# Kernel optimization log

Measured on AMD Instinct MI355X. Metric: run time of the kernel, lower is better.

Reference implementation:

```python
import jax, jax.numpy as jnp
import numpy as np

# ---- static physical configuration (matches init_kwargs param dict) ----
NX = NY = 513
NL = 3
N_ENS = 4
LX = LY = 5120.0e3
DX = LX / (NX - 1)
DY = LY / (NY - 1)
F0 = 9.375e-5
BETA = 1.754e-11
A2 = 0.0
A4 = 2.0e9
DELTA_EK = 2.0
TAU0 = 2.0e-5
BCCO = 0.2
ZFBC = BCCO / (1.0 + 0.5 * BCCO)
DT = 600.0
NUM_STEPS = 4
HEIGHTS = np.array([350.0, 750.0, 2900.0])
RED_G = np.array([0.025, 0.0125])

JAC_COEF = 1.0 / (F0 * DX * DY)
HYPERDIFF_COEF = A4 / F0**2 / DX**6
BOTTOM_FRICTION_COEF = DELTA_EK / (2.0 * abs(F0) * DX**2 * (-HEIGHTS[-1]))


def _build_constants():
    """Precompute stratification / mode / Helmholtz matrices (float64 numpy, cast to f32)."""
    A = np.zeros((NL, NL))
    A[0, 0] = 1.0 / (HEIGHTS[0] * RED_G[0])
    A[0, 1] = -1.0 / (HEIGHTS[0] * RED_G[0])
    for i in range(1, NL - 1):
        A[i, i - 1] = -1.0 / (HEIGHTS[i] * RED_G[i - 1])
        A[i, i] = 1.0 / HEIGHTS[i] * (1.0 / RED_G[i] + 1.0 / RED_G[i - 1])
        A[i, i + 1] = -1.0 / (HEIGHTS[i] * RED_G[i])
    A[-1, -1] = 1.0 / (HEIGHTS[NL - 1] * RED_G[NL - 2])
    A[-1, -2] = -1.0 / (HEIGHTS[NL - 1] * RED_G[NL - 2])
    lam_r, R = np.linalg.eig(A)
    lam_l, L = np.linalg.eig(A.T)
    lam_r, R, lam_l, L = lam_r.real, R.real, lam_l.real, L.real
    # align left eigenvectors with right eigenvalue ordering (biorthogonality)
    order = np.array([int(np.argmin(np.abs(lam_l - lr))) for lr in lam_r])
    L = L[:, order]
    Cl2m = np.diag(1.0 / np.diag(L.T @ R)) @ L.T
    Cm2l = R
    lambd = lam_r
    # DST-I eigenvalues of the 5-point Laplacian on the interior grid
    xg, yg = np.meshgrid(np.arange(1, NX - 1), np.arange(1, NY - 1), indexing='ij')
    lap_dst = (2 * (np.cos(np.pi / (NX - 1) * xg) - 1) / DX**2
               + 2 * (np.cos(np.pi / (NY - 1) * yg) - 1) / DY**2)
    helm_dst = lap_dst[None] / F0**2 - lambd[:, None, None]  # (nl, nx-2, ny-2)

    def np_dstI1D(x):
        N = x.shape[-1]
        xp = np.zeros(x.shape[:-1] + (N + 2,))
        xp[..., 1:-1] = x
        return np.fft.irfft(-1j * xp, n=2 * (N + 1), axis=-1, norm='ortho')[..., 1:N + 1]

    def np_dstI2D(x):
        return np.swapaxes(np_dstI1D(np.swapaxes(np_dstI1D(x), -1, -2)), -1, -2)

    const = np.ones((NL, NX, NY)) / (NX * NY)
    s = np.zeros_like(const)
    s[:, 1:-1, 1:-1] = np_dstI2D(np_dstI2D(const[:, 1:-1, 1:-1]) / helm_dst)
    hom_sol = (const + s * lambd[:, None, None])[:-1]  # (nl-1, nx, ny)
    M = (Cm2l[1:] - Cm2l[:-1])[:NL - 1, :NL - 1] * hom_sol.mean((1, 2))[None, :]
    alpha = -np.linalg.inv(M) @ (Cm2l[1:, :-1] - Cm2l[:-1, :-1])
    # wind forcing: curl(tau)/(f0*H1) on interior points; tau_y = 0, tau_x(y) only
    tau_x = -TAU0 * np.cos(2 * np.pi * (np.arange(NY) + 0.5) / NY)[None, :] * np.ones((NX, NY))
    dtaux_dy = (tau_x[1:-1, 2:] - tau_x[1:-1, :-2]) / (2 * DY)
    wind = (-dtaux_dy / (F0 * HEIGHTS[0]))[None]  # (1, nx-2, ny-2)
    f32 = lambda a: jnp.asarray(a, jnp.float32)
    return dict(A=f32(A), Cl2m=f32(Cl2m), Cm2l=f32(Cm2l), helmoltz_dst=f32(helm_dst),
                alpha_matrix=f32(alpha), homogeneous_sol=f32(hom_sol), wind_forcing=f32(wind))


# ---------------- stencil ops ----------------

def _pad11(x):
    return jnp.pad(x, [(0, 0)] * (x.ndim - 2) + [(1, 1), (1, 1)])


def laplacian_h_nobc(f):
    # unscaled 5-point Laplacian, interior values only: (..., nx-2, ny-2)
    return (f[..., 2:, 1:-1] + f[..., :-2, 1:-1] + f[..., 1:-1, 2:] + f[..., 1:-1, :-2]
            - 4.0 * f[..., 1:-1, 1:-1])


def laplacian_h(f, fc):
    # full-grid Laplacian with partial-slip boundary treatment (coefficient fc = zfbc)
    lap = _pad11(laplacian_h_nobc(f))
    lap = lap.at[..., 0, :].set(fc * (f[..., 1, :] - f[..., 0, :]))
    lap = lap.at[..., -1, :].set(fc * (f[..., -2, :] - f[..., -1, :]))
    lap = lap.at[..., :, 0].set(fc * (f[..., :, 1] - f[..., :, 0]))
    lap = lap.at[..., :, -1].set(fc * (f[..., :, -2] - f[..., :, -1]))
    return lap


def laplacian_h_boundaries(f, fc):
    # boundary Laplacian values, concat order: x=0 (y interior), x=-1, y=0 (full x), y=-1
    return jnp.concatenate([
        fc * (f[..., 1, 1:-1] - f[..., 0, 1:-1]),
        fc * (f[..., -2, 1:-1] - f[..., -1, 1:-1]),
        fc * (f[..., :, 1] - f[..., :, 0]),
        fc * (f[..., :, -2] - f[..., :, -1])], axis=-1)


def jacobi_h(f, g):
    # Arakawa 9-point Jacobian J(f, g), interior values (..., nx-2, ny-2)
    dx_f = f[..., 2:, :] - f[..., :-2, :]
    dx_g = g[..., 2:, :] - g[..., :-2, :]
    dy_f = f[..., 2:] - f[..., :-2]
    dy_g = g[..., 2:] - g[..., :-2]
    return ((dx_f[..., 1:-1] * dy_g[..., 1:-1, :] - dx_g[..., 1:-1] * dy_f[..., 1:-1, :])
            + (f[..., 2:, 1:-1] * dy_g[..., 2:, :] - f[..., :-2, 1:-1] * dy_g[..., :-2, :])
            - (f[..., 1:-1, 2:] * dx_g[..., 2:] - f[..., 1:-1, :-2] * dx_g[..., :-2])
            + (g[..., 1:-1, 2:] * dx_f[..., 2:] - g[..., 1:-1, :-2] * dx_f[..., :-2])
            - (g[..., 2:, 1:-1] * dy_f[..., 2:, :] - g[..., :-2, 1:-1] * dy_f[..., :-2, :])) / 12.0


# ---------------- DST-I elliptic solve ----------------

def dstI1D(x):
    N = x.shape[-1]
    z = jnp.zeros(x.shape[:-1] + (1,), x.dtype)
    xp = jnp.concatenate([z, x, z], axis=-1)
    return jnp.fft.irfft(-1j * xp.astype(jnp.complex64), n=2 * (N + 1), axis=-1,
                         norm='ortho')[..., 1:N + 1]


def dstI2D(x):
    return jnp.swapaxes(dstI1D(jnp.swapaxes(dstI1D(x), -1, -2)), -1, -2)


def inverse_elliptic_dst(f, op_dst):
    return dstI2D(dstI2D(f) / op_dst)


# ---------------- QG time derivative ----------------

def _time_derivatives(y, A, Cl2m, Cm2l, helm_dst, alpha, hom_sol, wind):
    q, p = y[0], y[1]  # (..., nl, nx, ny)
    # advection + hyperdiffusion RHS on interior (a_2 == 0 branch skipped as in source)
    rhs = JAC_COEF * jacobi_h(q, p)
    delta2_p = laplacian_h(p, ZFBC)
    rhs = rhs - HYPERDIFF_COEF * laplacian_h_nobc(laplacian_h(delta2_p, ZFBC))
    rhs = rhs.at[..., 0:1, :, :].add(wind)
    rhs = rhs.at[..., -1:, :, :].add(BOTTOM_FRICTION_COEF * laplacian_h_nobc(p[..., -1:, :, :]))
    dq = _pad11(rhs)
    # layers -> modes, DST Helmholtz inversion, homogeneous-solution correction
    rhs_h = jnp.einsum('ij,...jxy->...ixy', Cl2m, dq)
    dp_modes = _pad11(inverse_elliptic_dst(rhs_h[..., 1:-1, 1:-1], helm_dst))
    mean_m = dp_modes[..., :-1, :, :].mean((-2, -1))  # (..., nl-1)
    dalpha = jnp.einsum('ij,...j->...i', alpha, mean_m)[..., None, None]
    dp_modes = dp_modes.at[..., :-1, :, :].add(dalpha * hom_sol)
    dp = jnp.einsum('ij,...jxy->...ixy', Cm2l, dp_modes)
    # boundary vorticity update
    dp_bound = jnp.concatenate([dp[..., 0, 1:-1], dp[..., -1, 1:-1],
                                dp[..., :, 0], dp[..., :, -1]], axis=-1)
    delta_p_bound = laplacian_h_boundaries(dp / (F0 * DX)**2, ZFBC)
    dq_bound = delta_p_bound - jnp.einsum('ij,...jl->...il', A, dp_bound)
    ny2 = NY - 2
    dq = dq.at[..., 0, 1:-1].set(dq_bound[..., :ny2])
    dq = dq.at[..., -1, 1:-1].set(dq_bound[..., ny2:2 * ny2])
    dq = dq.at[..., :, 0].set(dq_bound[..., 2 * ny2:2 * ny2 + NX])
    dq = dq.at[..., :, -1].set(dq_bound[..., 2 * ny2 + NX:2 * ny2 + 2 * NX])
    return jnp.stack((dq, dp), 0)


def _forecast(y0, t, A, Cl2m, Cm2l, helm_dst, alpha, hom_sol, wind):
    deriv = lambda y: _time_derivatives(y, A, Cl2m, Cm2l, helm_dst, alpha, hom_sol, wind)

    def step(y, dt_):
        k1 = deriv(y)
        k2 = deriv(y + 0.5 * dt_ * k1)
        k3 = deriv(y + 0.5 * dt_ * k2)
        k4 = deriv(y + dt_ * k3)
        y_next = y + (dt_ / 6.0) * (k1 + 2.0 * k2 + 2.0 * k3 + k4)
        return y_next, y_next

    _, traj = jax.lax.scan(step, y0, t[1:] - t[:-1])
    return jnp.concatenate([y0[None], traj], axis=0)  # (T, 2, n_ens, nl, nx, ny)


def setup_inputs() -> dict:
    key = jax.random.key(0)
    y0 = 0.1 * jax.random.normal(key, (2, N_ENS, NL, NX, NY), dtype=jnp.float32)
    t = jnp.arange(NUM_STEPS + 1, dtype=jnp.float32) * DT
    consts = _build_constants()
    return dict(y0=y0, t=t, **consts)


def reference(y0, t, A, Cl2m, Cm2l, helmoltz_dst, alpha_matrix, homogeneous_sol, wind_forcing):
    return _forecast(y0, t, A, Cl2m, Cm2l, helmoltz_dst, alpha_matrix,
                     homogeneous_sol, wind_forcing)
```

## Files before the change

### kernel.cpp

```cpp
#include <hip/hip_runtime.h>
#include <math.h>

#define NXY 513
#define NIN 511
#define NL3 3
#define NE4 4
#define NB 12
#define GLD 512

static constexpr long FS  = (long)NE4 * NL3 * NXY * NXY;
static constexpr long GSZ = (long)NB * GLD * GLD;
static constexpr int  NSTEPS = 4;

static constexpr double dF0 = 9.375e-05;
static constexpr double dDX = 10000.0;
static constexpr float ZFBCf     = (float)(0.2 / (1.0 + 0.5 * 0.2));
static constexpr float JACCf     = (float)(1.0 / (dF0 * dDX * dDX));
static constexpr float HYPCf     = (float)(2.0e9 / (dF0 * dF0) / (dDX*dDX*dDX*dDX*dDX*dDX));
static constexpr float BFCf      = (float)(2.0 / (2.0 * dF0 * dDX * dDX * (-2900.0)));
static constexpr float INVF0DX2f = (float)(1.0 / ((dF0 * dDX) * (dF0 * dDX)));

typedef short  bf16x8 __attribute__((ext_vector_type(8)));
typedef float  f32x4  __attribute__((ext_vector_type(4)));
typedef unsigned int u32;
typedef __attribute__((address_space(1))) const u32 GAS;
typedef __attribute__((address_space(3))) u32 LAS;
#define GLDS(gp, lp) __builtin_amdgcn_global_load_lds((GAS*)(gp), (LAS*)(lp), 16, 0, 0)

__device__ __forceinline__ unsigned short f2bf(float x) {
    unsigned int u = __float_as_uint(x);
    return (unsigned short)((u + 0x7FFFu + ((u >> 16) & 1u)) >> 16);
}
__device__ __forceinline__ float bf2f(unsigned short h) {
    return __uint_as_float(((unsigned int)h) << 16);
}

__global__ void initS_kernel(unsigned short* __restrict__ Sh, unsigned short* __restrict__ Sl) {
    int k = blockIdx.x * 256 + threadIdx.x;
    int n = blockIdx.y;
    if (k >= GLD || n >= GLD) return;
    float v = 0.f;
    if (n < NIN && k < NIN) {
        int m = ((n + 1) * (k + 1)) & 1023;
        v = (float)(0.0625 * sin(M_PI * (double)m / 512.0));
    }
    unsigned short hs = f2bf(v);
    Sh[n * GLD + k] = hs;
    Sl[n * GLD + k] = f2bf(v - bf2f(hs));
}

__global__ __launch_bounds__(256) void fused_rhs_l2m(
    float* __restrict__ kq, unsigned short* __restrict__ Gh, unsigned short* __restrict__ Gl,
    const float* __restrict__ y, const float* __restrict__ wind, const float* __restrict__ Cl2m)
{
    __shared__ float ps[22][72];
    __shared__ float qs[22][72];
    __shared__ float l1[22][72];
    __shared__ float l2[22][72];
    const int e  = blockIdx.z;
    const int x0 = 1 + blockIdx.y * 16;
    const int y0 = 1 + blockIdx.x * 64;
    const int t  = threadIdx.x;
    const float* q = y;
    const float* p = y + FS;
    float rhs[4][3];

#define LAPBC(a, i, j, gx, gy) \
    ((gy) == 0       ? ZFBCf * (a[i][(j)+1] - a[i][j]) : \
     (gy) == NXY-1   ? ZFBCf * (a[i][(j)-1] - a[i][j]) : \
     (gx) == 0       ? ZFBCf * (a[(i)+1][j] - a[i][j]) : \
     (gx) == NXY-1   ? ZFBCf * (a[(i)-1][j] - a[i][j]) : \
     a[(i)+1][j] + a[(i)-1][j] + a[i][(j)+1] + a[i][(j)-1] - 4.f * a[i][j])

#pragma unroll
    for (int l = 0; l < 3; ++l) {
        __syncthreads();
        const int c = e * NL3 + l;
        const size_t off = (size_t)c * NXY * NXY;
        const float* pp = p + off;
        const float* qp = q + off;
        for (int idx = t; idx < 22 * 70; idx += 256) {
            int i = idx / 70, j = idx % 70;
            int gx = x0 - 3 + i, gy = y0 - 3 + j;
            bool in = (gx >= 0 && gx < NXY && gy >= 0 && gy < NXY);
            size_t go = (size_t)gx * NXY + gy;
            ps[i][j] = in ? pp[go] : 0.f;
            qs[i][j] = in ? qp[go] : 0.f;
        }
        __syncthreads();
        for (int idx = t; idx < 20 * 68; idx += 256) {
            int i = 1 + idx / 68, j = 1 + idx % 68;
            int gx = x0 - 3 + i, gy = y0 - 3 + j;
            float v = 0.f;
            if (gx >= 0 && gx < NXY && gy >= 0 && gy < NXY) v = LAPBC(ps, i, j, gx, gy);
            l1[i][j] = v;
        }
        __syncthreads();
        for (int idx = t; idx < 18 * 66; idx += 256) {
            int i = 2 + idx / 66, j = 2 + idx % 66;
            int gx = x0 - 3 + i, gy = y0 - 3 + j;
            float v = 0.f;
            if (gx >= 0 && gx < NXY && gy >= 0 && gy < NXY) v = LAPBC(l1, i, j, gx, gy);
            l2[i][j] = v;
        }
        __syncthreads();
#pragma unroll
        for (int u = 0; u < 4; ++u) {
            int idx = t + 256 * u;
            int i = 3 + idx / 64, j = 3 + idx % 64;
            int gx = x0 - 3 + i, gy = y0 - 3 + j;
            if (gx > NIN || gy > NIN) { rhs[u][l] = 0.f; continue; }
            float fmm=qs[i-1][j-1], fm0=qs[i-1][j], fmp=qs[i-1][j+1];
            float f0m=qs[i][j-1],                    f0p=qs[i][j+1];
            float fpm=qs[i+1][j-1], fp0=qs[i+1][j], fpp=qs[i+1][j+1];
            float gmm=ps[i-1][j-1], gm0=ps[i-1][j], gmp=ps[i-1][j+1];
            float g0m=ps[i][j-1],   g00=ps[i][j],   g0p=ps[i][j+1];
            float gpm=ps[i+1][j-1], gp0=ps[i+1][j], gpp=ps[i+1][j+1];
            float J1 = (fp0 - fm0) * (g0p - g0m) - (gp0 - gm0) * (f0p - f0m);
            float J2 = fp0 * (gpp - gpm) - fm0 * (gmp - gmm);
            float J3 = f0p * (gpp - gmp) - f0m * (gpm - gmm);
            float J4 = g0p * (fpp - fmp) - g0m * (fpm - fmm);
            float J5 = gp0 * (fpp - fpm) - gm0 * (fmp - fmm);
            float jac = (J1 + J2 - J3 + J4 - J5) * (1.0f / 12.0f);
            float lap3 = l2[i+1][j] + l2[i-1][j] + l2[i][j+1] + l2[i][j-1] - 4.f * l2[i][j];
            float v = JACCf * jac - HYPCf * lap3;
            if (l == 0)       v += wind[(size_t)(gx-1) * NIN + (gy-1)];
            if (l == NL3-1)   v += BFCf * (gp0 + gm0 + g0p + g0m - 4.f * g00);
            rhs[u][l] = v;
            kq[off + (size_t)gx * NXY + gy] = v;
        }
    }
#undef LAPBC

#pragma unroll
    for (int u = 0; u < 4; ++u) {
        int idx = t + 256 * u;
        int i = 3 + idx / 64, j = 3 + idx % 64;
        int gx = x0 - 3 + i, gy = y0 - 3 + j;
        size_t go = (size_t)(e * NL3) * GLD * GLD + (size_t)(gx-1) * GLD + (gy-1);
        if (gx > NIN || gy > NIN) {
#pragma unroll
            for (int m = 0; m < 3; ++m) {
                Gh[go + (size_t)m*GLD*GLD] = 0; Gl[go + (size_t)m*GLD*GLD] = 0;
            }
            continue;
        }
        float f0 = rhs[u][0], f1 = rhs[u][1], f2 = rhs[u][2];
        float v[3];
        v[0] = Cl2m[0]*f0 + Cl2m[1]*f1 + Cl2m[2]*f2;
        v[1] = Cl2m[3]*f0 + Cl2m[4]*f1 + Cl2m[5]*f2;
        v[2] = Cl2m[6]*f0 + Cl2m[7]*f1 + Cl2m[8]*f2;
#pragma unroll
        for (int m = 0; m < 3; ++m) {
            unsigned short hs = f2bf(v[m]);
            Gh[go + (size_t)m*GLD*GLD] = hs;
            Gl[go + (size_t)m*GLD*GLD] = f2bf(v[m] - bf2f(hs));
        }
    }
}

#define EPLD 68
__global__ __launch_bounds__(256, 3) void gemm_dst(
    const unsigned short* __restrict__ Ah, const unsigned short* __restrict__ Al,
    const unsigned short* __restrict__ Sh, const unsigned short* __restrict__ Sl,
    unsigned short* __restrict__ Ch, unsigned short* __restrict__ Cl,
    float* __restrict__ Cf, const float* __restrict__ helm, float* __restrict__ part)
{
    __shared__ __attribute__((aligned(16))) char ldsraw[32768];
    __shared__ float red[256];
    float* ep = (float*)ldsraw;
    const int id = blockIdx.x;
    const int nblk = id / 96, rr = id - nblk * 96;
    const int b = rr >> 3, mblk = rr & 7;
    const int m0 = mblk << 6, n0 = nblk << 6;
    const int t = threadIdx.x;
    const int wave = t >> 6, lane = t & 63;
    const int wr = wave >> 1, wc = wave & 1;
    const int lr = lane & 15, g = lane >> 4;
    const unsigned short* Abh = Ah + (size_t)b * 262144;
    const unsigned short* Abl = Al + (size_t)b * 262144;

    const int srow = t >> 2;
    const int scol = ((t & 3) ^ ((srow >> 1) & 3)) * 8;
    const size_t gAe = (size_t)(m0 + srow) * 512 + scol;
    const size_t gBe = (size_t)(n0 + srow) * 512 + scol;
    const int ldbase = wave * 1024;

    auto STAGE = [&](int buf, int kt) {
        char* bb = ldsraw + buf * 16384;
        int ke = kt * 32;
        GLDS(Abh + gAe + ke, bb + ldbase);
        GLDS(Abl + gAe + ke, bb + 4096 + ldbase);
        GLDS(Sh  + gBe + ke, bb + 8192 + ldbase);
        GLDS(Sl  + gBe + ke, bb + 12288 + ldbase);
    };

    f32x4 acc[2][2] = {};
    int abyte[2], bbyte[2];
#pragma unroll
    for (int i = 0; i < 2; ++i) {
        int ar = wr*32 + i*16 + lr;
        abyte[i] = ar*64 + ((g ^ ((ar >> 1) & 3)) * 16);
    }
#pragma unroll
    for (int j = 0; j < 2; ++j) {
        int br = wc*32 + j*16 + lr;
        bbyte[j] = 8192 + br*64 + ((g ^ ((br >> 1) & 3)) * 16);
    }

    STAGE(0, 0);
    __syncthreads();
    for (int it = 0; it < 16; ++it) {
        const int buf = it & 1;
        if (it < 15) STAGE(buf ^ 1, it + 1);
        const char* bb = ldsraw + buf * 16384;
        bf16x8 fbh[2], fbl[2];
#pragma unroll
        for (int j = 0; j < 2; ++j) {
            fbh[j] = *(const bf16x8*)(bb + bbyte[j]);
            fbl[j] = *(const bf16x8*)(bb + 4096 + bbyte[j]);
        }
#pragma unroll
        for (int i = 0; i < 2; ++i) {
            bf16x8 fah = *(const bf16x8*)(bb + abyte[i]);
            bf16x8 fal = *(const bf16x8*)(bb + 4096 + abyte[i]);
#pragma unroll
            for (int j = 0; j < 2; ++j) {
                acc[i][j] = __builtin_amdgcn_mfma_f32_16x16x32_bf16(fah, fbh[j], acc[i][j], 0, 0, 0);
                acc[i][j] = __builtin_amdgcn_mfma_f32_16x16x32_bf16(fah, fbl[j], acc[i][j], 0, 0, 0);
                acc[i][j] = __builtin_amdgcn_mfma_f32_16x16x32_bf16(fal, fbh[j], acc[i][j], 0, 0, 0);
            }
        }
        __syncthreads();
    }

    const int mode = b % NL3;
    const float* hp = helm ? (helm + (size_t)mode * NIN * NIN) : nullptr;
#pragma unroll
    for (int i = 0; i < 2; ++i) {
        int mml = wr*32 + i*16 + 4*g;
#pragma unroll
        for (int j = 0; j < 2; ++j) {
            int nnl = wc*32 + j*16 + lr;
            int nn = n0 + nnl;
            float v[4];
#pragma unroll
            for (int r = 0; r < 4; ++r) v[r] = acc[i][j][r];
            if (hp && nn < NIN) {
                int mmb = m0 + mml;
#pragma unroll
                for (int r = 0; r < 4; ++r)
                    if (mmb + r < NIN) v[r] /= hp[(size_t)nn*NIN + mmb + r];
            }
#pragma unroll
            for (int r = 0; r < 4; ++r) ep[nnl*EPLD + mml + r] = v[r];
        }
    }
    __syncthreads();

    float lsum = 0.f;
#pragma unroll
    for (int c = 0; c < 2; ++c) {
        int chunk = t + 256*c;
        int row = chunk >> 3;
        int cb  = (chunk & 7) * 8;
        float v[8];
#pragma unroll
        for (int k = 0; k < 8; ++k) v[k] = ep[row*EPLD + cb + k];
        size_t co = (size_t)b*262144 + (size_t)(n0 + row)*512 + m0 + cb;
        if (Cf) {
#pragma unroll
            for (int k = 0; k < 8; ++k) lsum += v[k];
            f32x4 v0 = {v[0], v[1], v[2], v[3]};
            f32x4 v1 = {v[4], v[5], v[6], v[7]};
            *(f32x4*)(Cf + co)     = v0;
            *(f32x4*)(Cf + co + 4) = v1;
        } else {
            unsigned int h[4], lo[4];
#pragma unroll
            for (int k = 0; k < 4; ++k) {
                unsigned short h0 = f2bf(v[2*k]), h1 = f2bf(v[2*k+1]);
                unsigned short l0 = f2bf(v[2*k]-bf2f(h0)), l1 = f2bf(v[2*k+1]-bf2f(h1));
                h[k]  = (unsigned int)h0 | ((unsigned int)h1 << 16);
                lo[k] = (unsigned int)l0 | ((unsigned int)l1 << 16);
            }
            *(uint4*)(Ch + co) = make_uint4(h[0], h[1], h[2], h[3]);
            *(uint4*)(Cl + co) = make_uint4(lo[0], lo[1], lo[2], lo[3]);
        }
    }

    if (part && mode < 2) {
        red[t] = lsum;
        __syncthreads();
        for (int w = 128; w >= 1; w >>= 1) {
            if (t < w) red[t] += red[t + w];
            __syncthreads();
        }
        if (t == 0) {
            int plane8 = (b / NL3) * 2 + mode;
            part[plane8 * 64 + nblk * 8 + mblk] = red[0];
        }
    }
}

__global__ __launch_bounds__(256) void m2l_mega(
    float* __restrict__ ynext, float* __restrict__ ytmp,
    const float* __restrict__ ycur, const float* __restrict__ kq,
    const float* __restrict__ G, const float* __restrict__ hom,
    const float* __restrict__ Cm2l, const float* __restrict__ Amat,
    const float* __restrict__ alpha, const float* __restrict__ part,
    const float* __restrict__ tarr, int s, float c1, float c2, int accumulate)
{
    __shared__ float sp[128];
    __shared__ float sdal[2];
    const int yy = blockIdx.x * 64 + threadIdx.x;
    const int xx = blockIdx.y * 4 + threadIdx.y;
    const int e  = blockIdx.z;
    const int tt = threadIdx.y * 64 + threadIdx.x;
    const bool act = (xx < NXY && yy < NXY);

    if (tt < 128) sp[tt] = part[(e*2 + (tt >> 6))*64 + (tt & 63)];
    __syncthreads();
    if (tt == 0) {
        float s0 = 0.f, s1 = 0.f;
        for (int j = 0; j < 64; ++j) { s0 += sp[j]; s1 += sp[64 + j]; }
        const float inv = 1.0f / ((float)NXY * (float)NXY);
        float mm0 = s0 * inv, mm1 = s1 * inv;
        sdal[0] = alpha[0]*mm0 + alpha[1]*mm1;
        sdal[1] = alpha[2]*mm0 + alpha[3]*mm1;
    }
    __syncthreads();
    if (!act) return;
    const float dal0 = sdal[0], dal1 = sdal[1];

    auto DP = [&](int px, int py, float* dp) {
        bool inter = (px >= 1 && px <= NIN && py >= 1 && py <= NIN);
        float mv0 = 0.f, mv1 = 0.f, mv2 = 0.f;
        if (inter) {
            size_t gb = (size_t)(e*NL3)*GLD*GLD + (size_t)(px-1)*GLD + (py-1);
            mv0 = G[gb]; mv1 = G[gb + (size_t)GLD*GLD]; mv2 = G[gb + 2*(size_t)GLD*GLD];
        }
        mv0 += dal0 * hom[(size_t)px*NXY + py];
        mv1 += dal1 * hom[(size_t)NXY*NXY + (size_t)px*NXY + py];
        dp[0] = Cm2l[0]*mv0 + Cm2l[1]*mv1 + Cm2l[2]*mv2;
        dp[1] = Cm2l[3]*mv0 + Cm2l[4]*mv1 + Cm2l[5]*mv2;
        dp[2] = Cm2l[6]*mv0 + Cm2l[7]*mv1 + Cm2l[8]*mv2;
    };

    float dp[3];
    DP(xx, yy, dp);

    const bool bnd = (xx == 0 || xx == NXY-1 || yy == 0 || yy == NXY-1);
    float kqv[3];
    if (!bnd) {
#pragma unroll
        for (int l = 0; l < 3; ++l)
            kqv[l] = kq[((size_t)(e*NL3 + l)*NXY + xx)*NXY + yy];
    } else {
        int xn, yn;
        if      (yy == 0)      { xn = xx;    yn = 1; }
        else if (yy == NXY-1)  { xn = xx;    yn = NXY-2; }
        else if (xx == 0)      { xn = 1;     yn = yy; }
        else                   { xn = NXY-2; yn = yy; }
        float dpn[3];
        DP(xn, yn, dpn);
#pragma unroll
        for (int l = 0; l < 3; ++l) {
            float lpb = ZFBCf * INVF0DX2f * (dpn[l] - dp[l]);
            kqv[l] = lpb - (Amat[l*3+0]*dp[0] + Amat[l*3+1]*dp[1] + Amat[l*3+2]*dp[2]);
        }
    }

    const float dt = tarr[s+1] - tarr[s];
    const float a1 = c1 * dt, a2 = c2 * dt;
#pragma unroll
    for (int l = 0; l < 3; ++l) {
        size_t oq = ((size_t)(e*NL3 + l)*NXY + xx)*NXY + yy;
        size_t op = oq + FS;
        float xq = ycur[oq], xp = ycur[op];
        float bq = accumulate ? ynext[oq] : xq;
        float bp = accumulate ? ynext[op] : xp;
        ynext[oq] = bq + a1 * kqv[l];
        ynext[op] = bp + a1 * dp[l];
        if (ytmp) {
            ytmp[oq] = xq + a2 * kqv[l];
            ytmp[op] = xp + a2 * dp[l];
        }
    }
}

__global__ void copy_kernel(float4* __restrict__ out, const float4* __restrict__ in, long n4) {
    for (long i = (long)blockIdx.x * blockDim.x + threadIdx.x; i < n4;
         i += (long)gridDim.x * blockDim.x)
        out[i] = in[i];
}

extern "C" void kernel_launch(void* const* d_in, const int* in_sizes, int n_in,
                              void* d_out, int out_size, void* d_ws, size_t ws_size,
                              hipStream_t stream) {
    const float* y0    = (const float*)d_in[0];
    const float* tarr  = (const float*)d_in[1];
    const float* Amat  = (const float*)d_in[2];
    const float* Cl2m  = (const float*)d_in[3];
    const float* Cm2l  = (const float*)d_in[4];
    const float* helm  = (const float*)d_in[5];
    const float* alpha = (const float*)d_in[6];
    const float* hom   = (const float*)d_in[7];
    const float* wind  = (const float*)d_in[8];
    float* out = (float*)d_out;
    char* base = (char*)d_ws;

    unsigned short* Sh = (unsigned short*)base;
    unsigned short* Sl = (unsigned short*)(base + 512*1024);
    float* ytmp = (float*)(base + 1024*1024);
    float* kq   = ytmp + 2*FS;
    char*  REGb = (char*)(kq + FS);
    unsigned short* P0h = (unsigned short*)REGb;
    unsigned short* P0l = P0h + GSZ;
    unsigned short* P1h = P0l + GSZ;
    unsigned short* P1l = P1h + GSZ;
    float* R4 = (float*)REGb;
    float* partial = (float*)(REGb + (size_t)2*FS*sizeof(float));

    const dim3 bSt(64, 4, 1);
    const dim3 gM(9, 129, NE4);
    const dim3 gF(8, 32, NE4);
    const dim3 gG(768, 1, 1);
    const long n4 = 2*FS/4;

    initS_kernel<<<dim3(2, GLD), 256, 0, stream>>>(Sh, Sl);
    copy_kernel<<<1024, 256, 0, stream>>>((float4*)out, (const float4*)y0, n4);

    auto evalstep = [&](const float* y, const float* ycur, float* ynext, float* otmp,
                        int s, float c1, float c2, int accumulate) {
        fused_rhs_l2m<<<gF, 256, 0, stream>>>(kq, P0h, P0l, y, wind, Cl2m);
        gemm_dst<<<gG, 256, 0, stream>>>(P0h, P0l, Sh, Sl, P1h, P1l, nullptr, nullptr, nullptr);
        gemm_dst<<<gG, 256, 0, stream>>>(P1h, P1l, Sh, Sl, P0h, P0l, nullptr, helm, nullptr);
        gemm_dst<<<gG, 256, 0, stream>>>(P0h, P0l, Sh, Sl, P1h, P1l, nullptr, nullptr, nullptr);
        gemm_dst<<<gG, 256, 0, stream>>>(P1h, P1l, Sh, Sl, nullptr, nullptr, R4, nullptr, partial);
        m2l_mega<<<gM, bSt, 0, stream>>>(ynext, otmp, ycur, kq, R4, hom, Cm2l, Amat,
                                         alpha, partial, tarr, s, c1, c2, accumulate);
    };

    for (int s = 0; s < NSTEPS; ++s) {
        float* ycur  = out + (size_t)s * 2 * FS;
        float* ynext = out + (size_t)(s + 1) * 2 * FS;
        evalstep(ycur, ycur, ynext, ytmp, s, 1.f/6.f, 0.5f, 0);
        evalstep(ytmp, ycur, ynext, ytmp, s, 2.f/6.f, 0.5f, 1);
        evalstep(ytmp, ycur, ynext, ytmp, s, 2.f/6.f, 1.0f, 1);
        evalstep(ytmp, ycur, ynext, nullptr, s, 1.f/6.f, 0.f, 1);
    }
}
```

Baseline: 2.352 ms.

## Split RHS and layer-to-mode kernels; triple-buffer GEMM LDS pipeline

```diff
diff --git a/kernel.cpp b/kernel.cpp
--- a/kernel.cpp
+++ b/kernel.cpp
@@ -49,21 +49,31 @@
     Sl[n * GLD + k] = f2bf(v - bf2f(hs));
 }
 
-__global__ __launch_bounds__(256) void fused_rhs_l2m(
-    float* __restrict__ kq, unsigned short* __restrict__ Gh, unsigned short* __restrict__ Gl,
-    const float* __restrict__ y, const float* __restrict__ wind, const float* __restrict__ Cl2m)
+__global__ __launch_bounds__(256) void fused_rhs(
+    float* __restrict__ kq, const float* __restrict__ q, const float* __restrict__ p,
+    const float* __restrict__ wind)
 {
     __shared__ float ps[22][72];
     __shared__ float qs[22][72];
     __shared__ float l1[22][72];
     __shared__ float l2[22][72];
-    const int e  = blockIdx.z;
+    const int c  = blockIdx.z;
     const int x0 = 1 + blockIdx.y * 16;
     const int y0 = 1 + blockIdx.x * 64;
     const int t  = threadIdx.x;
-    const float* q = y;
-    const float* p = y + FS;
-    float rhs[4][3];
+    const size_t off = (size_t)c * NXY * NXY;
+    const float* pp = p + off;
+    const float* qp = q + off;
+
+    for (int idx = t; idx < 22 * 70; idx += 256) {
+        int i = idx / 70, j = idx % 70;
+        int gx = x0 - 3 + i, gy = y0 - 3 + j;
+        bool in = (gx >= 0 && gx < NXY && gy >= 0 && gy < NXY);
+        size_t go = (size_t)gx * NXY + gy;
+        ps[i][j] = in ? pp[go] : 0.f;
+        qs[i][j] = in ? qp[go] : 0.f;
+    }
+    __syncthreads();
 
 #define LAPBC(a, i, j, gx, gy) \
     ((gy) == 0       ? ZFBCf * (a[i][(j)+1] - a[i][j]) : \
@@ -72,90 +82,73 @@
      (gx) == NXY-1   ? ZFBCf * (a[(i)-1][j] - a[i][j]) : \
      a[(i)+1][j] + a[(i)-1][j] + a[i][(j)+1] + a[i][(j)-1] - 4.f * a[i][j])
 
-#pragma unroll
-    for (int l = 0; l < 3; ++l) {
-        __syncthreads();
-        const int c = e * NL3 + l;
-        const size_t off = (size_t)c * NXY * NXY;
-        const float* pp = p + off;
-        const float* qp = q + off;
-        for (int idx = t; idx < 22 * 70; idx += 256) {
-            int i = idx / 70, j = idx % 70;
-            int gx = x0 - 3 + i, gy = y0 - 3 + j;
-            bool in = (gx >= 0 && gx < NXY && gy >= 0 && gy < NXY);
-            size_t go = (size_t)gx * NXY + gy;
-            ps[i][j] = in ? pp[go] : 0.f;
-            qs[i][j] = in ? qp[go] : 0.f;
-        }
-        __syncthreads();
-        for (int idx = t; idx < 20 * 68; idx += 256) {
-            int i = 1 + idx / 68, j = 1 + idx % 68;
-            int gx = x0 - 3 + i, gy = y0 - 3 + j;
-            float v = 0.f;
-            if (gx >= 0 && gx < NXY && gy >= 0 && gy < NXY) v = LAPBC(ps, i, j, gx, gy);
-            l1[i][j] = v;
-        }
-        __syncthreads();
-        for (int idx = t; idx < 18 * 66; idx += 256) {
-            int i = 2 + idx / 66, j = 2 + idx % 66;
-            int gx = x0 - 3 + i, gy = y0 - 3 + j;
-            float v = 0.f;
-            if (gx >= 0 && gx < NXY && gy >= 0 && gy < NXY) v = LAPBC(l1, i, j, gx, gy);
-            l2[i][j] = v;
-        }
-        __syncthreads();
-#pragma unroll
-        for (int u = 0; u < 4; ++u) {
-            int idx = t + 256 * u;
-            int i = 3 + idx / 64, j = 3 + idx % 64;
-            int gx = x0 - 3 + i, gy = y0 - 3 + j;
-            if (gx > NIN || gy > NIN) { rhs[u][l] = 0.f; continue; }
-            float fmm=qs[i-1][j-1], fm0=qs[i-1][j], fmp=qs[i-1][j+1];
-            float f0m=qs[i][j-1],                    f0p=qs[i][j+1];
-            float fpm=qs[i+1][j-1], fp0=qs[i+1][j], fpp=qs[i+1][j+1];
-            float gmm=ps[i-1][j-1], gm0=ps[i-1][j], gmp=ps[i-1][j+1];
-            float g0m=ps[i][j-1],   g00=ps[i][j],   g0p=ps[i][j+1];
-            float gpm=ps[i+1][j-1], gp0=ps[i+1][j], gpp=ps[i+1][j+1];
-            float J1 = (fp0 - fm0) * (g0p - g0m) - (gp0 - gm0) * (f0p - f0m);
-            float J2 = fp0 * (gpp - gpm) - fm0 * (gmp - gmm);
-            float J3 = f0p * (gpp - gmp) - f0m * (gpm - gmm);
-            float J4 = g0p * (fpp - fmp) - g0m * (fpm - fmm);
-            float J5 = gp0 * (fpp - fpm) - gm0 * (fmp - fmm);
-            float jac = (J1 + J2 - J3 + J4 - J5) * (1.0f / 12.0f);
-            float lap3 = l2[i+1][j] + l2[i-1][j] + l2[i][j+1] + l2[i][j-1] - 4.f * l2[i][j];
-            float v = JACCf * jac - HYPCf * lap3;
-            if (l == 0)       v += wind[(size_t)(gx-1) * NIN + (gy-1)];
-            if (l == NL3-1)   v += BFCf * (gp0 + gm0 + g0p + g0m - 4.f * g00);
-            rhs[u][l] = v;
-            kq[off + (size_t)gx * NXY + gy] = v;
-        }
-    }
+    for (int idx = t; idx < 20 * 68; idx += 256) {
+        int i = 1 + idx / 68, j = 1 + idx % 68;
+        int gx = x0 - 3 + i, gy = y0 - 3 + j;
+        float v = 0.f;
+        if (gx >= 0 && gx < NXY && gy >= 0 && gy < NXY) v = LAPBC(ps, i, j, gx, gy);
+        l1[i][j] = v;
+    }
+    __syncthreads();
+
+    for (int idx = t; idx < 18 * 66; idx += 256) {
+        int i = 2 + idx / 66, j = 2 + idx % 66;
+        int gx = x0 - 3 + i, gy = y0 - 3 + j;
+        float v = 0.f;
+        if (gx >= 0 && gx < NXY && gy >= 0 && gy < NXY) v = LAPBC(l1, i, j, gx, gy);
+        l2[i][j] = v;
+    }
+    __syncthreads();
 #undef LAPBC
 
-#pragma unroll
-    for (int u = 0; u < 4; ++u) {
-        int idx = t + 256 * u;
+    const int l = c % NL3;
+    for (int idx = t; idx < 16 * 64; idx += 256) {
         int i = 3 + idx / 64, j = 3 + idx % 64;
         int gx = x0 - 3 + i, gy = y0 - 3 + j;
-        size_t go = (size_t)(e * NL3) * GLD * GLD + (size_t)(gx-1) * GLD + (gy-1);
-        if (gx > NIN || gy > NIN) {
-#pragma unroll
-            for (int m = 0; m < 3; ++m) {
-                Gh[go + (size_t)m*GLD*GLD] = 0; Gl[go + (size_t)m*GLD*GLD] = 0;
-            }
-            continue;
-        }
-        float f0 = rhs[u][0], f1 = rhs[u][1], f2 = rhs[u][2];
-        float v[3];
-        v[0] = Cl2m[0]*f0 + Cl2m[1]*f1 + Cl2m[2]*f2;
-        v[1] = Cl2m[3]*f0 + Cl2m[4]*f1 + Cl2m[5]*f2;
-        v[2] = Cl2m[6]*f0 + Cl2m[7]*f1 + Cl2m[8]*f2;
-#pragma unroll
-        for (int m = 0; m < 3; ++m) {
-            unsigned short hs = f2bf(v[m]);
-            Gh[go + (size_t)m*GLD*GLD] = hs;
-            Gl[go + (size_t)m*GLD*GLD] = f2bf(v[m] - bf2f(hs));
-        }
+        if (gx > NIN || gy > NIN) continue;
+        float fmm=qs[i-1][j-1], fm0=qs[i-1][j], fmp=qs[i-1][j+1];
+        float f0m=qs[i][j-1],                    f0p=qs[i][j+1];
+        float fpm=qs[i+1][j-1], fp0=qs[i+1][j], fpp=qs[i+1][j+1];
+        float gmm=ps[i-1][j-1], gm0=ps[i-1][j], gmp=ps[i-1][j+1];
+        float g0m=ps[i][j-1],   g00=ps[i][j],   g0p=ps[i][j+1];
+        float gpm=ps[i+1][j-1], gp0=ps[i+1][j], gpp=ps[i+1][j+1];
+        float J1 = (fp0 - fm0) * (g0p - g0m) - (gp0 - gm0) * (f0p - f0m);
+        float J2 = fp0 * (gpp - gpm) - fm0 * (gmp - gmm);
+        float J3 = f0p * (gpp - gmp) - f0m * (gpm - gmm);
+        float J4 = g0p * (fpp - fmp) - g0m * (fpm - fmm);
+        float J5 = gp0 * (fpp - fpm) - gm0 * (fmp - fmm);
+        float jac = (J1 + J2 - J3 + J4 - J5) * (1.0f / 12.0f);
+        float lap3 = l2[i+1][j] + l2[i-1][j] + l2[i][j+1] + l2[i][j-1] - 4.f * l2[i][j];
+        float v = JACCf * jac - HYPCf * lap3;
+        if (l == 0)       v += wind[(size_t)(gx-1) * NIN + (gy-1)];
+        if (l == NL3-1)   v += BFCf * (gp0 + gm0 + g0p + g0m - 4.f * g00);
+        kq[off + (size_t)gx * NXY + gy] = v;
+    }
+}
+
+__global__ void l2m_kernel(unsigned short* __restrict__ Gh, unsigned short* __restrict__ Gl,
+                           const float* __restrict__ kq, const float* __restrict__ Cl2m) {
+    int ry = blockIdx.x * blockDim.x + threadIdx.x;
+    int rx = blockIdx.y * blockDim.y + threadIdx.y;
+    int e = blockIdx.z;
+    size_t go = (size_t)(e * NL3) * GLD * GLD + (size_t)rx * GLD + ry;
+    if (rx >= NIN || ry >= NIN) {
+        for (int i = 0; i < 3; ++i) { Gh[go + (size_t)i*GLD*GLD] = 0; Gl[go + (size_t)i*GLD*GLD] = 0; }
+        return;
+    }
+    size_t base = ((size_t)(e * NL3) * NXY + (rx + 1)) * NXY + (ry + 1);
+    float f0 = kq[base];
+    float f1 = kq[base + (size_t)NXY*NXY];
+    float f2 = kq[base + 2*(size_t)NXY*NXY];
+    float v[3];
+    v[0] = Cl2m[0]*f0 + Cl2m[1]*f1 + Cl2m[2]*f2;
+    v[1] = Cl2m[3]*f0 + Cl2m[4]*f1 + Cl2m[5]*f2;
+    v[2] = Cl2m[6]*f0 + Cl2m[7]*f1 + Cl2m[8]*f2;
+#pragma unroll
+    for (int i = 0; i < 3; ++i) {
+        unsigned short hs = f2bf(v[i]);
+        Gh[go + (size_t)i*GLD*GLD] = hs;
+        Gl[go + (size_t)i*GLD*GLD] = f2bf(v[i] - bf2f(hs));
     }
 }
 
@@ -166,7 +159,7 @@
     unsigned short* __restrict__ Ch, unsigned short* __restrict__ Cl,
     float* __restrict__ Cf, const float* __restrict__ helm, float* __restrict__ part)
 {
-    __shared__ __attribute__((aligned(16))) char ldsraw[32768];
+    __shared__ __attribute__((aligned(16))) char ldsraw[49152];
     __shared__ float red[256];
     float* ep = (float*)ldsraw;
     const int id = blockIdx.x;
@@ -209,10 +202,12 @@
     }
 
     STAGE(0, 0);
-    __syncthreads();
+    STAGE(1, 1);
+    asm volatile("s_waitcnt vmcnt(4)" ::: "memory");
+    __builtin_amdgcn_s_barrier();
     for (int it = 0; it < 16; ++it) {
-        const int buf = it & 1;
-        if (it < 15) STAGE(buf ^ 1, it + 1);
+        const int buf = it % 3;
+        if (it < 14) STAGE((it + 2) % 3, it + 2);
         const char* bb = ldsraw + buf * 16384;
         bf16x8 fbh[2], fbl[2];
 #pragma unroll
@@ -231,8 +226,11 @@
                 acc[i][j] = __builtin_amdgcn_mfma_f32_16x16x32_bf16(fal, fbh[j], acc[i][j], 0, 0, 0);
             }
         }
-        __syncthreads();
-    }
+        if (it < 13)      asm volatile("s_waitcnt vmcnt(4)" ::: "memory");
+        else              asm volatile("s_waitcnt vmcnt(0)" ::: "memory");
+        __builtin_amdgcn_s_barrier();
+    }
+    __syncthreads();
 
     const int mode = b % NL3;
     const float* hp = helm ? (helm + (size_t)mode * NIN * NIN) : nullptr;
@@ -424,7 +422,8 @@
 
     const dim3 bSt(64, 4, 1);
     const dim3 gM(9, 129, NE4);
-    const dim3 gF(8, 32, NE4);
+    const dim3 gF(8, 32, NB);
+    const dim3 gL2M(8, 128, NE4);
     const dim3 gG(768, 1, 1);
     const long n4 = 2*FS/4;
 
@@ -433,7 +432,8 @@
 
     auto evalstep = [&](const float* y, const float* ycur, float* ynext, float* otmp,
                         int s, float c1, float c2, int accumulate) {
-        fused_rhs_l2m<<<gF, 256, 0, stream>>>(kq, P0h, P0l, y, wind, Cl2m);
+        fused_rhs<<<gF, 256, 0, stream>>>(kq, y, y + FS, wind);
+        l2m_kernel<<<gL2M, bSt, 0, stream>>>(P0h, P0l, kq, Cl2m);
         gemm_dst<<<gG, 256, 0, stream>>>(P0h, P0l, Sh, Sl, P1h, P1l, nullptr, nullptr, nullptr);
         gemm_dst<<<gG, 256, 0, stream>>>(P1h, P1l, Sh, Sl, P0h, P0l, nullptr, helm, nullptr);
         gemm_dst<<<gG, 256, 0, stream>>>(P0h, P0l, Sh, Sl, P1h, P1l, nullptr, nullptr, nullptr);
```

Measured after the change: 2.392 ms. Within noise of the previous version (+1.7%).
